# Kernel tuning notes

Measured on AMD Instinct MI355X. Metric: run time of the kernel, lower is better.

## Reference

```python
import jax, jax.numpy as jnp
import numpy as np

B, N, NEV, E, D, L = 4, 20000, 100000, 400000, 64, 3

def setup_inputs() -> dict:
    key = jax.random.key(0)
    ks = jax.random.split(key, 12)
    x = jax.random.normal(ks[0], (B, N, 3), dtype=jnp.float32)
    # channel 0 is the susceptible boolean mask (0/1)
    mask0 = (jax.random.uniform(ks[1], (B, N)) < 0.3).astype(jnp.float32)
    x = x.at[..., 0].set(mask0)
    dag_edge_index = jax.random.randint(ks[2], (2, E), 0, NEV, dtype=jnp.int64)
    event_to_node = jax.random.randint(ks[3], (NEV,), 0, N, dtype=jnp.int64)
    event_src_node = jax.random.randint(ks[4], (NEV,), 0, N, dtype=jnp.int64)
    s = 1.0 / np.sqrt(D)
    Wp = jax.random.normal(ks[5], (6, D), dtype=jnp.float32) * (1.0 / np.sqrt(6))
    bp = jnp.zeros((D,), dtype=jnp.float32)
    Ws = jax.random.normal(ks[6], (L, D, D), dtype=jnp.float32) * s
    Wa = jax.random.normal(ks[7], (L, D, D), dtype=jnp.float32) * s
    ba = jnp.zeros((L, D), dtype=jnp.float32)
    Wo = jax.random.normal(ks[8], (D,), dtype=jnp.float32) * s
    bo = jnp.zeros((), dtype=jnp.float32)
    return {"x": x, "Wp": Wp, "bp": bp, "Ws": Ws, "Wa": Wa, "ba": ba,
            "Wo": Wo, "bo": bo, "dag_edge_index": dag_edge_index,
            "event_to_node": event_to_node, "event_src_node": event_src_node}

def reference(x, Wp, bp, Ws, Wa, ba, Wo, bo, dag_edge_index, event_to_node, event_src_node):
    n_events = event_src_node.shape[0]
    # event features: [B, n_events, 6] -> project -> ReLU
    ev_feat = jnp.concatenate([x[:, event_src_node, :], x[:, event_to_node, :]], axis=-1)
    h = jax.nn.relu(ev_feat @ Wp + bp)  # [B, n_events, D]
    # reversed DAG edges: src = dag[1], dst = dag[0]
    src_e, dst_e = dag_edge_index[1], dag_edge_index[0]
    deg = jnp.zeros((n_events,), h.dtype).at[dst_e].add(1.0)
    deg = jnp.maximum(deg, 1.0)[None, :, None]
    for l in range(Ws.shape[0]):
        agg = jnp.zeros_like(h).at[:, dst_e].add(h[:, src_e])  # scatter-add mean agg
        h = jax.nn.relu(h @ Ws[l] + (agg / deg) @ Wa[l] + ba[l])
    # aggregate events back to nodes (mean)
    node_emb = jnp.zeros((x.shape[0], x.shape[1], h.shape[-1]), h.dtype).at[:, event_to_node].add(h)
    count = jnp.zeros((x.shape[1],), h.dtype).at[event_to_node].add(1.0)
    node_emb = node_emb / jnp.maximum(count, 1.0)[None, :, None]
    scores = node_emb @ Wo + bo  # [B, N]
    susceptible = x[..., 0] > 0
    scores = jnp.where(susceptible, -jnp.inf, scores)
    return jax.nn.log_softmax(scores, axis=-1)
```

## Files before the change

### kernel.cpp

```cpp
#include <hip/hip_runtime.h>
#include <hip/hip_bf16.h>
#include <math.h>

constexpr int B   = 4;
constexpr int N   = 20000;
constexpr int NEV = 100000;
constexpr int E   = 400000;
constexpr int D   = 64;
constexpr int L   = 3;
constexpr int XS  = 136;
constexpr int CAP = 32;
constexpr int CHUNK = 625;

typedef short  short8 __attribute__((ext_vector_type(8)));
typedef float  f32x4  __attribute__((ext_vector_type(4)));
typedef float  f32x2  __attribute__((ext_vector_type(2)));


__device__ inline unsigned short f2bu(float f) {
  union { __hip_bfloat16 b; unsigned short s; } u;
  u.b = __float2bfloat16(f);
  return u.s;
}
__device__ inline unsigned packbf(float lo, float hi) {
  return ((unsigned)f2bu(hi) << 16) | (unsigned)f2bu(lo);
}


__global__ void k_zero(float4* __restrict__ p, int n4) {
  int i = blockIdx.x * blockDim.x + threadIdx.x;
  if (i < n4) p[i] = make_float4(0.f, 0.f, 0.f, 0.f);
}

__global__ void k_prep(const int* __restrict__ dag,
                       int* __restrict__ cnt,
                       int* __restrict__ csrc,
                       const int* __restrict__ e2n,
                       int* __restrict__ ncount,
                       const float* __restrict__ Ws,
                       const float* __restrict__ Wa,
                       unsigned short* __restrict__ Wt) {
  int bid = blockIdx.x;
  if (bid < 1563) {
    int i = bid * 256 + threadIdx.x;
    if (i < E) {
      int dst = dag[i];
      int src = dag[E + i];
      int pos = atomicAdd(&cnt[dst], 1);
      if (pos < CAP) csrc[dst * CAP + pos] = src;
    }
  } else if (bid < 1954) {
    int i = (bid - 1563) * 256 + threadIdx.x;
    if (i < NEV) atomicAdd(&ncount[e2n[i]], 1);
  } else {
    int i = (bid - 1954) * 256 + threadIdx.x;
    int l = i >> 13;
    int r = i & 8191;
    int n = r >> 7;
    int s = r & 127;
    int sl = (s < 64) ? s : s - 64;
    int c  = (sl & 3) * 16 + (sl >> 2);
    float v = (s < 64) ? Ws[l * 4096 + c * 64 + n]
                       : Wa[l * 4096 + c * 64 + n];
    Wt[l * 8192 + n * 128 + s] = f2bu(v);
  }
}

__global__ __launch_bounds__(256) void k_proj(const float* __restrict__ x,
                                              const float* __restrict__ Wp,
                                              const float* __restrict__ bp,
                                              const int* __restrict__ esrc,
                                              const int* __restrict__ e2n,
                                              unsigned* __restrict__ h,
                                              float* __restrict__ nscore) {
  int gid = blockIdx.x * blockDim.x + threadIdx.x;
  if (gid < B * N) nscore[gid] = 0.f;
  const int lane = threadIdx.x & 63;
  const int e    = gid >> 6;
  int sn = esrc[e], tn = e2n[e];
  float xval = 0.f;
  if (lane < 24) {
    int bl = lane / 6, rem = lane % 6;
    int node = (rem < 3) ? sn : tn;
    xval = x[(size_t)(bl * N + node) * 3 + (rem < 3 ? rem : rem - 3)];
  }
  const int b = lane >> 4, p = lane & 15;
  float xv[6];
#pragma unroll
  for (int k = 0; k < 6; ++k) xv[k] = __shfl(xval, b * 6 + k, 64);
  float a[4];
#pragma unroll
  for (int t = 0; t < 4; ++t) {
    int d = p + 16 * t;
    float acc = bp[d];
#pragma unroll
    for (int k = 0; k < 6; ++k) acc += xv[k] * Wp[k * 64 + d];
    a[t] = fmaxf(acc, 0.f);
  }
  int w = __builtin_amdgcn_cvt_pk_fp8_f32(a[0], a[1], 0, false);
  w     = __builtin_amdgcn_cvt_pk_fp8_f32(a[2], a[3], w, true);
  h[e * 64 + lane] = (unsigned)w;
}

template <bool LAST>
__global__ __launch_bounds__(256, 8) void k_layer(
    const unsigned short* __restrict__ Wt,
    const float* __restrict__ ba,
    const float* __restrict__ Wo,
    const int* __restrict__ e2n,
    const int* __restrict__ cnt,
    const int* __restrict__ csrc,
    const unsigned char* __restrict__ h_in,
    unsigned char* __restrict__ h_out,
    float* __restrict__ nscore) {
  __shared__ unsigned short sX[64 * XS];
  const int tid  = threadIdx.x;
  const int wv   = tid >> 6, lane = tid & 63;
  const int e0   = blockIdx.x * 16;
  const int r0   = e0 * 4;

  const int qg = lane >> 4, sub = lane & 15;
  int vidx = csrc[(size_t)(e0 + wv * 4 + qg) * CAP + sub];
  int c_l  = cnt[e0 + wv * 4 + (lane & 3)];

  {
    uint4 v = *(const uint4*)(h_in + (size_t)r0 * 64 + tid * 16);
    int row = tid >> 2, ch = tid & 3;
    unsigned vv[4] = {v.x, v.y, v.z, v.w};
    unsigned out[8];
#pragma unroll
    for (int i = 0; i < 4; ++i) {
      f32x2 lo = __builtin_amdgcn_cvt_pk_f32_fp8((int)vv[i], false);
      f32x2 hi = __builtin_amdgcn_cvt_pk_f32_fp8((int)vv[i], true);
      out[2 * i]     = packbf(lo[0], lo[1]);
      out[2 * i + 1] = packbf(hi[0], hi[1]);
    }
    unsigned short* dst = sX + row * XS + ch * 16;
    *(uint4*)dst       = *(uint4*)&out[0];
    *(uint4*)(dst + 8) = *(uint4*)&out[4];
  }

#pragma unroll
  for (int ei = 0; ei < 4; ++ei) {
    int c = __shfl(c_l, ei, 64);
    int cc16 = min(c, 16);
    float a[16];
#pragma unroll
    for (int i = 0; i < 16; ++i) a[i] = 0.f;
    for (int p = 0; p < cc16; p += 4) {
      int j = p + qg;
      if (j < cc16) {
        int s = __shfl(vidx, ei * 16 + j, 64);
        uint4 v = *(const uint4*)(h_in + (size_t)s * 256 + sub * 16);
        unsigned vv[4] = {v.x, v.y, v.z, v.w};
#pragma unroll
        for (int i = 0; i < 4; ++i) {
          f32x2 lo = __builtin_amdgcn_cvt_pk_f32_fp8((int)vv[i], false);
          f32x2 hi = __builtin_amdgcn_cvt_pk_f32_fp8((int)vv[i], true);
          a[4 * i + 0] += lo[0]; a[4 * i + 1] += lo[1];
          a[4 * i + 2] += hi[0]; a[4 * i + 3] += hi[1];
        }
      }
    }
    int cc = min(c, CAP);
    for (int j = 16 + qg; j < cc; j += 4) {
      int s = csrc[(size_t)(e0 + wv * 4 + ei) * CAP + j];
      uint4 v = *(const uint4*)(h_in + (size_t)s * 256 + sub * 16);
      unsigned vv[4] = {v.x, v.y, v.z, v.w};
#pragma unroll
      for (int i = 0; i < 4; ++i) {
        f32x2 lo = __builtin_amdgcn_cvt_pk_f32_fp8((int)vv[i], false);
        f32x2 hi = __builtin_amdgcn_cvt_pk_f32_fp8((int)vv[i], true);
        a[4 * i + 0] += lo[0]; a[4 * i + 1] += lo[1];
        a[4 * i + 2] += hi[0]; a[4 * i + 3] += hi[1];
      }
    }
#pragma unroll
    for (int i = 0; i < 16; ++i) {
      a[i] += __shfl_xor(a[i], 16, 64);
      a[i] += __shfl_xor(a[i], 32, 64);
    }
    if (qg == 0) {
      float inv = 1.f / fmaxf((float)c, 1.f);
      int lrow = (wv * 4 + ei) * 4 + (sub >> 2);
      unsigned out[8];
#pragma unroll
      for (int i = 0; i < 8; ++i)
        out[i] = packbf(a[2 * i] * inv, a[2 * i + 1] * inv);
      unsigned short* dst = sX + lrow * XS + 64 + (sub & 3) * 16;
      *(uint4*)dst       = *(uint4*)&out[0];
      *(uint4*)(dst + 8) = *(uint4*)&out[4];
    }
  }
  __syncthreads();

  const int m = lane & 15, q = lane >> 4;
  f32x4 acc[4];
#pragma unroll
  for (int t = 0; t < 4; ++t) {
    float bv = ba[t * 16 + m];
    acc[t] = (f32x4){bv, bv, bv, bv};
  }
  const unsigned short* xbase = sX + (wv * 16 + m) * XS + q * 8;
  const unsigned short* wbase = Wt + m * 128 + q * 8;
#pragma unroll
  for (int kk = 0; kk < 4; ++kk) {
    short8 av = *(const short8*)(xbase + kk * 32);
#pragma unroll
    for (int t = 0; t < 4; ++t) {
      short8 bv = *(const short8*)(wbase + t * 2048 + kk * 32);
      acc[t] = __builtin_amdgcn_mfma_f32_16x16x32_bf16(av, bv, acc[t], 0, 0, 0);
    }
  }

  if constexpr (!LAST) {
#pragma unroll
    for (int r = 0; r < 4; ++r) {
      int w = __builtin_amdgcn_cvt_pk_fp8_f32(fmaxf(acc[0][r], 0.f),
                                              fmaxf(acc[1][r], 0.f), 0, false);
      w     = __builtin_amdgcn_cvt_pk_fp8_f32(fmaxf(acc[2][r], 0.f),
                                              fmaxf(acc[3][r], 0.f), w, true);
      int grow = r0 + wv * 16 + q * 4 + r;
      ((unsigned*)h_out)[grow * 16 + m] = (unsigned)w;
    }
  } else {
    float w0 = Wo[m], w1 = Wo[16 + m], w2 = Wo[32 + m], w3 = Wo[48 + m];
#pragma unroll
    for (int r = 0; r < 4; ++r) {
      float v = fmaxf(acc[0][r], 0.f) * w0 + fmaxf(acc[1][r], 0.f) * w1
              + fmaxf(acc[2][r], 0.f) * w2 + fmaxf(acc[3][r], 0.f) * w3;
      v += __shfl_xor(v, 1, 64);
      v += __shfl_xor(v, 2, 64);
      v += __shfl_xor(v, 4, 64);
      v += __shfl_xor(v, 8, 64);
      if (m == 0) {
        int grow = r0 + wv * 16 + q * 4 + r;
        int e = grow >> 2, b = grow & 3;
        atomicAdd(&nscore[b * N + e2n[e]], v);
      }
    }
  }
}

__device__ inline float ls_score(const float* nscore, const int* ncount,
                                 const float* x, float bov, int b, int n) {
  return (x[(size_t)(b * N + n) * 3] > 0.f)
             ? -INFINITY
             : nscore[b * N + n] / fmaxf((float)ncount[n], 1.f) + bov;
}

__global__ __launch_bounds__(256) void k_ls1(const float* __restrict__ nscore,
                                             const int* __restrict__ ncount,
                                             const float* __restrict__ x,
                                             const float* __restrict__ bo,
                                             float* __restrict__ pmax,
                                             float* __restrict__ psum,
                                             float* __restrict__ sc) {
  const int b = blockIdx.x >> 5, ch = blockIdx.x & 31;
  const int n0 = ch * CHUNK;
  const int tid = threadIdx.x;
  const float bov = bo[0];
  float s0 = -INFINITY, s1 = -INFINITY, s2 = -INFINITY;
  if (tid < CHUNK) {
    s0 = ls_score(nscore, ncount, x, bov, b, n0 + tid);
    sc[b * N + n0 + tid] = s0;
  }
  if (tid + 256 < CHUNK) {
    s1 = ls_score(nscore, ncount, x, bov, b, n0 + tid + 256);
    sc[b * N + n0 + tid + 256] = s1;
  }
  if (tid + 512 < CHUNK) {
    s2 = ls_score(nscore, ncount, x, bov, b, n0 + tid + 512);
    sc[b * N + n0 + tid + 512] = s2;
  }
  float m = fmaxf(fmaxf(s0, s1), s2);
  __shared__ float red[4];
#pragma unroll
  for (int o = 32; o; o >>= 1) m = fmaxf(m, __shfl_xor(m, o, 64));
  if ((tid & 63) == 0) red[tid >> 6] = m;
  __syncthreads();
  float pm = fmaxf(fmaxf(red[0], red[1]), fmaxf(red[2], red[3]));
  float pm2 = (pm == -INFINITY) ? 0.f : pm;
  float e = expf(s0 - pm2) + expf(s1 - pm2) + expf(s2 - pm2);
#pragma unroll
  for (int o = 32; o; o >>= 1) e += __shfl_xor(e, o, 64);
  __syncthreads();
  if ((tid & 63) == 0) red[tid >> 6] = e;
  __syncthreads();
  if (tid == 0) {
    pmax[blockIdx.x] = pm;
    psum[blockIdx.x] = red[0] + red[1] + red[2] + red[3];
  }
}

__global__ __launch_bounds__(256) void k_ls3(const float* __restrict__ pmax,
                                             const float* __restrict__ psum,
                                             const float* __restrict__ sc,
                                             float* __restrict__ out) {
  const int b = blockIdx.x >> 5, ch = blockIdx.x & 31;
  const int n0 = ch * CHUNK;
  const int tid = threadIdx.x;
  __shared__ float sgm, slse;
  if (tid < 64) {
    float pm = (tid < 32) ? pmax[b * 32 + tid] : -INFINITY;
    float ps = (tid < 32) ? psum[b * 32 + tid] : 0.f;
    float gm = pm;
#pragma unroll
    for (int o = 32; o; o >>= 1) gm = fmaxf(gm, __shfl_xor(gm, o, 64));
    float gm2 = (gm == -INFINITY) ? 0.f : gm;
    float c = (pm == -INFINITY) ? 0.f : ps * expf(pm - gm2);
#pragma unroll
    for (int o = 32; o; o >>= 1) c += __shfl_xor(c, o, 64);
    if (tid == 0) { sgm = gm; slse = logf(c); }
  }
  __syncthreads();
  const float gm = sgm, lse = slse;
  for (int i = tid; i < CHUNK; i += 256) {
    int n = n0 + i;
    out[b * N + n] = fmaxf(sc[b * N + n] - gm - lse, -3.0e38f);
  }
}

extern "C" void kernel_launch(void* const* d_in, const int* in_sizes, int n_in,
                              void* d_out, int out_size, void* d_ws, size_t ws_size,
                              hipStream_t stream) {
  const float* x   = (const float*)d_in[0];
  const float* Wp  = (const float*)d_in[1];
  const float* bp  = (const float*)d_in[2];
  const float* Ws  = (const float*)d_in[3];
  const float* Wa  = (const float*)d_in[4];
  const float* ba  = (const float*)d_in[5];
  const float* Wo  = (const float*)d_in[6];
  const float* bo  = (const float*)d_in[7];
  const int*   dag = (const int*)d_in[8];
  const int*   e2n = (const int*)d_in[9];
  const int*   esr = (const int*)d_in[10];

  int*   ws     = (int*)d_ws;
  int*   cnt    = ws;
  int*   ncount = ws + 100000;
  float* nscore = (float*)(ws + 120000);
  float* pmax   = (float*)(ws + 200000);
  float* psum   = (float*)(ws + 200128);
  int*   csrc   = ws + 200704;
  unsigned short* Wt = (unsigned short*)(ws + 3400704);
  unsigned char* h0 = (unsigned char*)(ws + 3406912);
  unsigned char* h1 = h0 + (size_t)B * NEV * D;
  float* sc     = (float*)(h1 + (size_t)B * NEV * D);
  float* out    = (float*)d_out;

  k_zero<<<(30000 + 255) / 256, 256, 0, stream>>>((float4*)ws, 30000);
  k_prep<<<2050, 256, 0, stream>>>(dag, cnt, csrc, e2n, ncount, Ws, Wa, Wt);
  k_proj<<<(B * NEV * 16) / 256, 256, 0, stream>>>(x, Wp, bp, esr, e2n,
                                                   (unsigned*)h0, nscore);

  k_layer<false><<<NEV / 16, 256, 0, stream>>>(Wt,         ba,       Wo, e2n,
                                               cnt, csrc, h0, h1, nscore);
  k_layer<false><<<NEV / 16, 256, 0, stream>>>(Wt + 8192,  ba + D,   Wo, e2n,
                                               cnt, csrc, h1, h0, nscore);
  k_layer<true><<<NEV / 16, 256, 0, stream>>>(Wt + 16384,  ba + 2*D, Wo, e2n,
                                              cnt, csrc, h0, h1, nscore);

  k_ls1<<<B * 32, 256, 0, stream>>>(nscore, ncount, x, bo, pmax, psum, sc);
  k_ls3<<<B * 32, 256, 0, stream>>>(pmax, psum, sc, out);
}
```

Measured before the change: 334.2 us.

## Build MFMA operands directly in registers, dropping LDS staging in layer kernel

```diff
diff --git a/kernel.cpp b/kernel.cpp
--- a/kernel.cpp
+++ b/kernel.cpp
@@ -8,7 +8,6 @@
 constexpr int E   = 400000;
 constexpr int D   = 64;
 constexpr int L   = 3;
-constexpr int XS  = 136;
 constexpr int CAP = 32;
 constexpr int CHUNK = 625;
 
@@ -24,6 +23,32 @@
 }
 __device__ inline unsigned packbf(float lo, float hi) {
   return ((unsigned)f2bu(hi) << 16) | (unsigned)f2bu(lo);
+}
+__device__ inline void cvt16(float* a, uint4 v) {
+  unsigned vv[4] = {v.x, v.y, v.z, v.w};
+#pragma unroll
+  for (int i = 0; i < 4; ++i) {
+    f32x2 lo = __builtin_amdgcn_cvt_pk_f32_fp8((int)vv[i], false);
+    f32x2 hi = __builtin_amdgcn_cvt_pk_f32_fp8((int)vv[i], true);
+    a[4 * i + 0] = lo[0]; a[4 * i + 1] = lo[1];
+    a[4 * i + 2] = hi[0]; a[4 * i + 3] = hi[1];
+  }
+}
+__device__ inline void add16(float* a, uint4 v) {
+  unsigned vv[4] = {v.x, v.y, v.z, v.w};
+#pragma unroll
+  for (int i = 0; i < 4; ++i) {
+    f32x2 lo = __builtin_amdgcn_cvt_pk_f32_fp8((int)vv[i], false);
+    f32x2 hi = __builtin_amdgcn_cvt_pk_f32_fp8((int)vv[i], true);
+    a[4 * i + 0] += lo[0]; a[4 * i + 1] += lo[1];
+    a[4 * i + 2] += hi[0]; a[4 * i + 3] += hi[1];
+  }
+}
+__device__ inline short8 pack8(const float* f) {
+  union { unsigned u[4]; short8 s; } r;
+#pragma unroll
+  for (int i = 0; i < 4; ++i) r.u[i] = packbf(f[2 * i], f[2 * i + 1]);
+  return r.s;
 }
 
 
@@ -54,15 +79,16 @@
     if (i < NEV) atomicAdd(&ncount[e2n[i]], 1);
   } else {
     int i = (bid - 1954) * 256 + threadIdx.x;
-    int l = i >> 13;
-    int r = i & 8191;
-    int n = r >> 7;
-    int s = r & 127;
-    int sl = (s < 64) ? s : s - 64;
-    int c  = (sl & 3) * 16 + (sl >> 2);
-    float v = (s < 64) ? Ws[l * 4096 + c * 64 + n]
-                       : Wa[l * 4096 + c * 64 + n];
-    Wt[l * 8192 + n * 128 + s] = f2bu(v);
+    int l  = i >> 13;
+    int r  = i & 8191;
+    int n  = r >> 7;
+    int s2 = r & 127;
+    int hf = s2 >> 6, s = s2 & 63;
+    int b  = ((s >> 3) & 3) * 16 + (s >> 5) * 8 + (s & 7);
+    int c  = (b & 3) * 16 + (b >> 2);
+    float v = hf ? Wa[l * 4096 + c * 64 + n]
+                 : Ws[l * 4096 + c * 64 + n];
+    Wt[l * 8192 + n * 128 + s2] = f2bu(v);
   }
 }
 
@@ -113,104 +139,73 @@
     const unsigned char* __restrict__ h_in,
     unsigned char* __restrict__ h_out,
     float* __restrict__ nscore) {
-  __shared__ unsigned short sX[64 * XS];
   const int tid  = threadIdx.x;
   const int wv   = tid >> 6, lane = tid & 63;
   const int e0   = blockIdx.x * 16;
   const int r0   = e0 * 4;
-
-  const int qg = lane >> 4, sub = lane & 15;
-  int vidx = csrc[(size_t)(e0 + wv * 4 + qg) * CAP + sub];
-  int c_l  = cnt[e0 + wv * 4 + (lane & 3)];
-
+  const int m    = lane & 15, q = lane >> 4;
+  const int el   = m >> 2;
+  const int bb   = m & 3;
+  const int e_loc = wv * 4 + el;
+
+  int vidx = csrc[(size_t)(e0 + wv * 4 + q) * CAP + m];
+
+  uint4 vd = *(const uint4*)(h_in + (size_t)(r0 + wv * 16 + m) * 64 + q * 16);
+
+  int c    = cnt[e0 + e_loc];
+  int cc   = min(c, CAP);
+  int cc16 = min(cc, 16);
+  float a[16];
+#pragma unroll
+  for (int i = 0; i < 16; ++i) a[i] = 0.f;
+  const unsigned char* gb = h_in + bb * 64 + q * 16;
+  for (int p = 0; p < cc16; p += 4) {
+    uint4 v[4];
+#pragma unroll
+    for (int t = 0; t < 4; ++t) {
+      v[t] = make_uint4(0u, 0u, 0u, 0u);
+      int j = p + t;
+      int s = __shfl(vidx, (el << 4) | (j & 15), 64);
+      if (j < cc16) v[t] = *(const uint4*)(gb + (size_t)s * 256);
+    }
+#pragma unroll
+    for (int t = 0; t < 4; ++t) add16(a, v[t]);
+  }
+  for (int j = 16; j < cc; ++j) {
+    int s = csrc[(size_t)(e0 + e_loc) * CAP + j];
+    add16(a, *(const uint4*)(gb + (size_t)s * 256));
+  }
   {
-    uint4 v = *(const uint4*)(h_in + (size_t)r0 * 64 + tid * 16);
-    int row = tid >> 2, ch = tid & 3;
-    unsigned vv[4] = {v.x, v.y, v.z, v.w};
-    unsigned out[8];
-#pragma unroll
-    for (int i = 0; i < 4; ++i) {
-      f32x2 lo = __builtin_amdgcn_cvt_pk_f32_fp8((int)vv[i], false);
-      f32x2 hi = __builtin_amdgcn_cvt_pk_f32_fp8((int)vv[i], true);
-      out[2 * i]     = packbf(lo[0], lo[1]);
-      out[2 * i + 1] = packbf(hi[0], hi[1]);
-    }
-    unsigned short* dst = sX + row * XS + ch * 16;
-    *(uint4*)dst       = *(uint4*)&out[0];
-    *(uint4*)(dst + 8) = *(uint4*)&out[4];
-  }
-
-#pragma unroll
-  for (int ei = 0; ei < 4; ++ei) {
-    int c = __shfl(c_l, ei, 64);
-    int cc16 = min(c, 16);
-    float a[16];
-#pragma unroll
-    for (int i = 0; i < 16; ++i) a[i] = 0.f;
-    for (int p = 0; p < cc16; p += 4) {
-      int j = p + qg;
-      if (j < cc16) {
-        int s = __shfl(vidx, ei * 16 + j, 64);
-        uint4 v = *(const uint4*)(h_in + (size_t)s * 256 + sub * 16);
-        unsigned vv[4] = {v.x, v.y, v.z, v.w};
-#pragma unroll
-        for (int i = 0; i < 4; ++i) {
-          f32x2 lo = __builtin_amdgcn_cvt_pk_f32_fp8((int)vv[i], false);
-          f32x2 hi = __builtin_amdgcn_cvt_pk_f32_fp8((int)vv[i], true);
-          a[4 * i + 0] += lo[0]; a[4 * i + 1] += lo[1];
-          a[4 * i + 2] += hi[0]; a[4 * i + 3] += hi[1];
-        }
-      }
-    }
-    int cc = min(c, CAP);
-    for (int j = 16 + qg; j < cc; j += 4) {
-      int s = csrc[(size_t)(e0 + wv * 4 + ei) * CAP + j];
-      uint4 v = *(const uint4*)(h_in + (size_t)s * 256 + sub * 16);
-      unsigned vv[4] = {v.x, v.y, v.z, v.w};
-#pragma unroll
-      for (int i = 0; i < 4; ++i) {
-        f32x2 lo = __builtin_amdgcn_cvt_pk_f32_fp8((int)vv[i], false);
-        f32x2 hi = __builtin_amdgcn_cvt_pk_f32_fp8((int)vv[i], true);
-        a[4 * i + 0] += lo[0]; a[4 * i + 1] += lo[1];
-        a[4 * i + 2] += hi[0]; a[4 * i + 3] += hi[1];
-      }
-    }
-#pragma unroll
-    for (int i = 0; i < 16; ++i) {
-      a[i] += __shfl_xor(a[i], 16, 64);
-      a[i] += __shfl_xor(a[i], 32, 64);
-    }
-    if (qg == 0) {
-      float inv = 1.f / fmaxf((float)c, 1.f);
-      int lrow = (wv * 4 + ei) * 4 + (sub >> 2);
-      unsigned out[8];
-#pragma unroll
-      for (int i = 0; i < 8; ++i)
-        out[i] = packbf(a[2 * i] * inv, a[2 * i + 1] * inv);
-      unsigned short* dst = sX + lrow * XS + 64 + (sub & 3) * 16;
-      *(uint4*)dst       = *(uint4*)&out[0];
-      *(uint4*)(dst + 8) = *(uint4*)&out[4];
-    }
-  }
-  __syncthreads();
-
-  const int m = lane & 15, q = lane >> 4;
+    float inv = 1.f / fmaxf((float)c, 1.f);
+#pragma unroll
+    for (int i = 0; i < 16; ++i) a[i] *= inv;
+  }
+  short8 ag0 = pack8(a), ag1 = pack8(a + 8);
+
+  short8 ad0, ad1;
+  {
+    float fd[16];
+    cvt16(fd, vd);
+    ad0 = pack8(fd); ad1 = pack8(fd + 8);
+  }
+
   f32x4 acc[4];
 #pragma unroll
   for (int t = 0; t < 4; ++t) {
     float bv = ba[t * 16 + m];
     acc[t] = (f32x4){bv, bv, bv, bv};
   }
-  const unsigned short* xbase = sX + (wv * 16 + m) * XS + q * 8;
-  const unsigned short* wbase = Wt + m * 128 + q * 8;
-#pragma unroll
-  for (int kk = 0; kk < 4; ++kk) {
-    short8 av = *(const short8*)(xbase + kk * 32);
-#pragma unroll
-    for (int t = 0; t < 4; ++t) {
-      short8 bv = *(const short8*)(wbase + t * 2048 + kk * 32);
-      acc[t] = __builtin_amdgcn_mfma_f32_16x16x32_bf16(av, bv, acc[t], 0, 0, 0);
-    }
+  const unsigned short* wb = Wt + m * 128 + q * 8;
+#pragma unroll
+  for (int t = 0; t < 4; ++t) {
+    acc[t] = __builtin_amdgcn_mfma_f32_16x16x32_bf16(
+        ad0, *(const short8*)(wb + t * 2048 + 0),  acc[t], 0, 0, 0);
+    acc[t] = __builtin_amdgcn_mfma_f32_16x16x32_bf16(
+        ad1, *(const short8*)(wb + t * 2048 + 32), acc[t], 0, 0, 0);
+    acc[t] = __builtin_amdgcn_mfma_f32_16x16x32_bf16(
+        ag0, *(const short8*)(wb + t * 2048 + 64), acc[t], 0, 0, 0);
+    acc[t] = __builtin_amdgcn_mfma_f32_16x16x32_bf16(
+        ag1, *(const short8*)(wb + t * 2048 + 96), acc[t], 0, 0, 0);
   }
 
   if constexpr (!LAST) {
```

After: 558.2 us. 1.67x slower.
